# Performance work log

Measured on AMD Instinct MI355X. Metric: run time of the kernel, lower is better.

The kernel has to match this reference:

```python
import jax, jax.numpy as jnp
import numpy as np

N = 100000
E = 1600000
IN = 128
H = 256
K = 7          # n_hops + 1
INTERVAL = 3
R = K - INTERVAL + 1  # n_relations + 1 = 5


def setup_inputs() -> dict:
    key = jax.random.key(0)
    ks = jax.random.split(key, 8)
    features = jax.random.normal(ks[0], (N, IN), dtype=jnp.float32)
    W1 = jax.random.normal(ks[1], (K, IN, H), dtype=jnp.float32) * (1.0 / np.sqrt(IN))
    b1 = jnp.zeros((K, H), dtype=jnp.float32)
    W2 = jax.random.normal(ks[2], (K, H, H), dtype=jnp.float32) * (1.0 / np.sqrt(H))
    b2 = jnp.zeros((K, H), dtype=jnp.float32)
    Wr = jax.random.normal(ks[3], (R, H * INTERVAL, H), dtype=jnp.float32) * (1.0 / np.sqrt(H * INTERVAL))
    br = jnp.zeros((R, H), dtype=jnp.float32)
    row = jax.random.randint(ks[4], (E,), 0, N, dtype=jnp.int64)
    col = jax.random.randint(ks[5], (E,), 0, N, dtype=jnp.int64)
    return {"features": features, "W1": W1, "b1": b1, "W2": W2, "b2": b2,
            "Wr": Wr, "br": br, "row": row, "col": col}


def _norm_adj(row, col):
    # set_diag=True: add self loops; symm_norm: D^-1/2 (A+I) D^-1/2
    diag = jnp.arange(N, dtype=row.dtype)
    r = jnp.concatenate([row, diag])
    c = jnp.concatenate([col, diag])
    deg = jax.ops.segment_sum(jnp.ones_like(r, dtype=jnp.float32), r, num_segments=N)
    dinv = jnp.where(deg > 0, jax.lax.rsqrt(deg), 0.0)
    w = dinv[r] * dinv[c]  # [E+N]
    return r, c, w


def _forward(features, W1, b1, W2, b2, Wr, br, row, col):
    r, c, w = _norm_adj(row, col)

    def spmm(x):  # x: [N, F] -> A_hat @ x
        return jax.ops.segment_sum(x[c] * w[:, None], r, num_segments=N)

    def step(x, _):
        nx = spmm(x)
        return nx, nx

    _, hops = jax.lax.scan(step, features, None, length=K - 1)  # [K-1, N, IN]
    hop_feats = jnp.concatenate([features[None], hops], axis=0)  # [K, N, IN]

    # per-hop DeepSets (2-layer MLP with ReLU): [K, N, H]
    h = jax.nn.relu(jnp.einsum('kni,kih->knh', hop_feats, W1) + b1[:, None, :])
    h = jnp.einsum('knh,khg->kng', h, W2) + b2[:, None, :]

    hops_feats = jnp.transpose(h, (1, 0, 2))  # [N, K, H]
    # sliding windows of INTERVAL hops: [R, N, INTERVAL*H]
    wins = jnp.stack([hops_feats[:, i:i + INTERVAL, :].reshape(N, INTERVAL * H)
                      for i in range(R)], axis=0)
    rel = jax.nn.relu(jnp.einsum('rnd,rdh->rnh', wins, Wr) + br[:, None, :])  # [R, N, H]
    out = jnp.transpose(rel, (1, 0, 2)).reshape(N, R * H)  # concat over relations
    return out


def reference(features, W1, b1, W2, b2, Wr, br, row, col):
    return _forward(features, W1, b1, W2, b2, Wr, br, row, col)
```

## Files before the change

kernel.cpp:

```cpp
#include <hip/hip_runtime.h>

#define N_NODES 100000
#define E_EDGES 1600000
#define IN_F 128
#define H_F 256
#define K_HOPS 7
#define R_REL 5
#define OUT_W (R_REL * H_F)

typedef __attribute__((ext_vector_type(8))) short short8;
typedef __attribute__((ext_vector_type(4))) float f32x4;

#define GLOAD16(g, l) __builtin_amdgcn_global_load_lds( \
    (const __attribute__((address_space(1))) void*)(g), \
    (__attribute__((address_space(3))) void*)(l), 16, 0, 0)


__global__ void zero_int(int* __restrict__ p, int n) {
    int t = blockIdx.x * blockDim.x + threadIdx.x;
    if (t < n) p[t] = 0;
}

__global__ void deg_count(const int* __restrict__ row, int* __restrict__ deg) {
    int e = blockIdx.x * blockDim.x + threadIdx.x;
    if (e < E_EDGES) atomicAdd(&deg[row[e]], 1);
}

__global__ void dinv_compute(const int* __restrict__ deg, float* __restrict__ dinv) {
    int i = blockIdx.x * blockDim.x + threadIdx.x;
    if (i < N_NODES) dinv[i] = rsqrtf((float)(deg[i] + 1));
}

__global__ __launch_bounds__(1024) void exscan_rowptr(const int* __restrict__ deg,
                                                      int* __restrict__ rowptr) {
    __shared__ int wsum[16];
    __shared__ int carry_s;
    const int t = threadIdx.x, lane = t & 63, wv = t >> 6;
    if (t == 0) carry_s = 0;
    __syncthreads();
    for (int base = 0; base < N_NODES; base += 1024) {
        int i = base + t;
        int v = (i < N_NODES) ? deg[i] : 0;
        int x = v;
#pragma unroll
        for (int off = 1; off < 64; off <<= 1) {
            int n = __shfl_up(x, off, 64);
            if (lane >= off) x += n;
        }
        if (lane == 63) wsum[wv] = x;
        __syncthreads();
        if (wv == 0 && lane < 16) {
            int s = wsum[lane];
#pragma unroll
            for (int off = 1; off < 16; off <<= 1) {
                int n = __shfl_up(s, off, 64);
                if (lane >= off) s += n;
            }
            wsum[lane] = s;
        }
        __syncthreads();
        int wbase = (wv == 0) ? 0 : wsum[wv - 1];
        if (i < N_NODES) rowptr[i] = carry_s + wbase + x - v;
        __syncthreads();
        if (t == 1023) carry_s += wsum[15];
        __syncthreads();
    }
    if (threadIdx.x == 0) rowptr[N_NODES] = carry_s;
}

__global__ void csr_scatter(const int* __restrict__ row, const int* __restrict__ col,
                            const float* __restrict__ dinv, const int* __restrict__ rowptr,
                            int* __restrict__ cursor, int* __restrict__ cols2,
                            float* __restrict__ ew) {
    int e = blockIdx.x * blockDim.x + threadIdx.x;
    if (e >= E_EDGES) return;
    int r = row[e], c = col[e];
    int pos = rowptr[r] + atomicAdd(&cursor[r], 1);
    cols2[pos] = c;
    ew[pos] = dinv[r] * dinv[c];
}

__global__ __launch_bounds__(256) void spmm_csr(
    const float2* __restrict__ x, const int* __restrict__ rowptr,
    const int* __restrict__ cols, const float* __restrict__ w,
    const float* __restrict__ dinv, float2* __restrict__ y) {
    const int wave = threadIdx.x >> 6, lane = threadIdx.x & 63;
    const int i = blockIdx.x * 4 + wave;
    if (i >= N_NODES) return;
    const float d = dinv[i];
    float2 xv = x[(size_t)i * 64 + lane];
    float2 acc;
    acc.x = d * d * xv.x;
    acc.y = d * d * xv.y;
    int j = rowptr[i];
    const int e = rowptr[i + 1];
    for (; j + 3 < e; j += 4) {
        int c0 = cols[j], c1 = cols[j + 1], c2 = cols[j + 2], c3 = cols[j + 3];
        float w0 = w[j], w1 = w[j + 1], w2 = w[j + 2], w3 = w[j + 3];
        float2 v0 = x[(size_t)c0 * 64 + lane];
        float2 v1 = x[(size_t)c1 * 64 + lane];
        float2 v2 = x[(size_t)c2 * 64 + lane];
        float2 v3 = x[(size_t)c3 * 64 + lane];
        acc.x += w0 * v0.x + w1 * v1.x + w2 * v2.x + w3 * v3.x;
        acc.y += w0 * v0.y + w1 * v1.y + w2 * v2.y + w3 * v3.y;
    }
    for (; j < e; ++j) {
        int c0 = cols[j];
        float w0 = w[j];
        float2 v0 = x[(size_t)c0 * 64 + lane];
        acc.x += w0 * v0.x;
        acc.y += w0 * v0.y;
    }
    y[(size_t)i * 64 + lane] = acc;
}


__device__ __forceinline__ void f2bf_split(float v, short& h, short& l) {
    unsigned u = __float_as_uint(v);
    unsigned hb = (u + 0x7FFFu + ((u >> 16) & 1u)) >> 16;
    float fh = __uint_as_float(hb << 16);
    float r = v - fh;
    unsigned u2 = __float_as_uint(r);
    unsigned lb = (u2 + 0x7FFFu + ((u2 >> 16) & 1u)) >> 16;
    h = (short)(unsigned short)hb;
    l = (short)(unsigned short)lb;
}

__global__ __launch_bounds__(256) void wc_compute(const float* __restrict__ W2,
                                                  const float* __restrict__ Wr,
                                                  float* __restrict__ Wc) {
    const int z = blockIdx.x, j = blockIdx.y, g = threadIdx.x;
    const int r = z / 3, d = z % 3, hop = r + d;
    const float* a = W2 + (size_t)hop * H_F * H_F + (size_t)j * H_F;
    const float* b = Wr + ((size_t)r * 768 + (size_t)d * H_F) * H_F + g;
    float acc = 0.f;
#pragma unroll 4
    for (int h = 0; h < H_F; ++h) acc += a[h] * b[(size_t)h * H_F];
    Wc[(size_t)z * H_F * H_F + (size_t)j * H_F + g] = acc;
}

__global__ __launch_bounds__(256) void bc_compute(const float* __restrict__ b2,
                                                  const float* __restrict__ Wr,
                                                  const float* __restrict__ br,
                                                  float* __restrict__ bc) {
    const int r = blockIdx.x, g = threadIdx.x;
    float acc = br[(size_t)r * H_F + g];
    for (int t = 0; t < 3 * H_F; ++t) {
        float bv = b2[(size_t)(r + t / H_F) * H_F + (t % H_F)];
        acc += bv * Wr[((size_t)r * 768 + t) * H_F + g];
    }
    bc[(size_t)r * H_F + g] = acc;
}

__global__ void transpose_convert(const float* __restrict__ in, short* __restrict__ oh,
                                  short* __restrict__ ol, int Kd, int grp) {
    __shared__ float t[32][33];
    const int i0 = blockIdx.x * 32, n0 = blockIdx.y * 32, z = blockIdx.z;
    const int tx = threadIdx.x, ty = threadIdx.y;
    const int outLd = grp * Kd;
    const float* ip = in + (size_t)z * Kd * 256;
#pragma unroll
    for (int j = 0; j < 4; ++j)
        t[ty + 8 * j][tx] = ip[(size_t)(i0 + ty + 8 * j) * 256 + n0 + tx];
    __syncthreads();
    size_t base = (size_t)(z / grp) * 256 * outLd + (size_t)(z % grp) * Kd;
#pragma unroll
    for (int j = 0; j < 4; ++j) {
        float v = t[tx][ty + 8 * j];
        short hb, lb;
        f2bf_split(v, hb, lb);
        size_t o = base + (size_t)(n0 + ty + 8 * j) * outLd + i0 + tx;
        oh[o] = hb;
        ol[o] = lb;
    }
}


#define LROW 40

__global__ __launch_bounds__(256, 2) void gemm_mlp(
    const float* __restrict__ A,
    const short* __restrict__ BTh, const short* __restrict__ BTl,
    short* __restrict__ Ch, short* __restrict__ Cl,
    const float* __restrict__ bias, int M)
{
    __shared__ short lds_buf[4 * 128 * LROW];
    short* Ah = lds_buf;
    short* Al = lds_buf + 128 * LROW;
    short* Bh = lds_buf + 2 * 128 * LROW;
    short* Bl = lds_buf + 3 * 128 * LROW;

    const int tid = threadIdx.x;
    const int lane = tid & 63, wave = tid >> 6;
    const int wm = wave & 1, wn = wave >> 1;
    const int fr = lane & 15, fg = lane >> 4;
    const int m0 = blockIdx.y * 128;
    const int n0 = blockIdx.x * 128;

    const int sr = tid >> 1;
    const int sc = (tid & 1) * 16;
    const bool avalid = (m0 + sr) < M;
    const int arow = avalid ? (m0 + sr) : (M - 1);

    f32x4 ga[4];
    short8 gbh[2], gbl[2];
    {
        const float* ap = A + (size_t)arow * IN_F + sc;
        const short* bph = BTh + (size_t)(n0 + sr) * IN_F + sc;
        const short* bpl = BTl + (size_t)(n0 + sr) * IN_F + sc;
#pragma unroll
        for (int l = 0; l < 4; ++l) ga[l] = *(const f32x4*)(ap + 4 * l);
        gbh[0] = *(const short8*)bph;  gbh[1] = *(const short8*)(bph + 8);
        gbl[0] = *(const short8*)bpl;  gbl[1] = *(const short8*)(bpl + 8);
    }

    f32x4 acc[4][4];
#pragma unroll
    for (int i = 0; i < 4; ++i)
#pragma unroll
        for (int j = 0; j < 4; ++j) acc[i][j] = (f32x4)0.f;

    const int nk = IN_F / 32;
    for (int kk = 0; kk < nk; ++kk) {
        __syncthreads();
        {
            short8 vh[2], vl[2];
#pragma unroll
            for (int l = 0; l < 4; ++l) {
                f32x4 v = ga[l];
                if (!avalid) v = (f32x4)0.f;
#pragma unroll
                for (int e = 0; e < 4; ++e) {
                    short hb, lb;
                    f2bf_split(v[e], hb, lb);
                    vh[l >> 1][(l & 1) * 4 + e] = hb;
                    vl[l >> 1][(l & 1) * 4 + e] = lb;
                }
            }
            *(short8*)(Ah + sr * LROW + sc)     = vh[0];
            *(short8*)(Ah + sr * LROW + sc + 8) = vh[1];
            *(short8*)(Al + sr * LROW + sc)     = vl[0];
            *(short8*)(Al + sr * LROW + sc + 8) = vl[1];
            *(short8*)(Bh + sr * LROW + sc)     = gbh[0];
            *(short8*)(Bh + sr * LROW + sc + 8) = gbh[1];
            *(short8*)(Bl + sr * LROW + sc)     = gbl[0];
            *(short8*)(Bl + sr * LROW + sc + 8) = gbl[1];
        }
        __syncthreads();

        if (kk + 1 < nk) {
            int k0 = (kk + 1) * 32;
            const float* ap = A + (size_t)arow * IN_F + k0 + sc;
            const short* bph = BTh + (size_t)(n0 + sr) * IN_F + k0 + sc;
            const short* bpl = BTl + (size_t)(n0 + sr) * IN_F + k0 + sc;
#pragma unroll
            for (int l = 0; l < 4; ++l) ga[l] = *(const f32x4*)(ap + 4 * l);
            gbh[0] = *(const short8*)bph;  gbh[1] = *(const short8*)(bph + 8);
            gbl[0] = *(const short8*)bpl;  gbl[1] = *(const short8*)(bpl + 8);
        }

        short8 afh[4], afl[4], bfh[4], bfl[4];
#pragma unroll
        for (int mf = 0; mf < 4; ++mf) {
            int r = wm * 64 + mf * 16 + fr;
            afh[mf] = *(const short8*)(Ah + r * LROW + fg * 8);
            afl[mf] = *(const short8*)(Al + r * LROW + fg * 8);
        }
#pragma unroll
        for (int nf = 0; nf < 4; ++nf) {
            int r = wn * 64 + nf * 16 + fr;
            bfh[nf] = *(const short8*)(Bh + r * LROW + fg * 8);
            bfl[nf] = *(const short8*)(Bl + r * LROW + fg * 8);
        }
#pragma unroll
        for (int mf = 0; mf < 4; ++mf)
#pragma unroll
            for (int nf = 0; nf < 4; ++nf) {
                acc[mf][nf] = __builtin_amdgcn_mfma_f32_16x16x32_bf16(
                    afh[mf], bfh[nf], acc[mf][nf], 0, 0, 0);
                acc[mf][nf] = __builtin_amdgcn_mfma_f32_16x16x32_bf16(
                    afh[mf], bfl[nf], acc[mf][nf], 0, 0, 0);
                acc[mf][nf] = __builtin_amdgcn_mfma_f32_16x16x32_bf16(
                    afl[mf], bfh[nf], acc[mf][nf], 0, 0, 0);
            }
    }

#pragma unroll
    for (int nf = 0; nf < 4; ++nf) {
        int colg = n0 + wn * 64 + nf * 16 + fr;
        float bv = bias[colg];
#pragma unroll
        for (int mf = 0; mf < 4; ++mf) {
            int rowbase = m0 + wm * 64 + mf * 16 + fg * 4;
#pragma unroll
            for (int j = 0; j < 4; ++j) {
                int rowg = rowbase + j;
                if (rowg < M) {
                    float v = fmaxf(acc[mf][nf][j] + bv, 0.f);
                    short hb, lb;
                    f2bf_split(v, hb, lb);
                    size_t idx = (size_t)rowg * H_F + colg;
                    Ch[idx] = hb;
                    Cl[idx] = lb;
                }
            }
        }
    }
}


__global__ __launch_bounds__(256, 2) void gemm_rel(
    const short* __restrict__ h1h, const short* __restrict__ h1l, long hopStride,
    const short* __restrict__ wch, const short* __restrict__ wcl,
    float* __restrict__ outB, const float* __restrict__ bcB, int M)
{
    __shared__ short lds[2][4][128 * 32];

    const int tid = threadIdx.x;
    const int lane = tid & 63, wave = tid >> 6;
    const int wm = wave & 1, wn = wave >> 1;
    const int fr = lane & 15, fg = lane >> 4;
    const int m0 = blockIdx.y * 128;
    const int n0 = blockIdx.x * 128;
    const int rrel = blockIdx.z;

    const short* Agh = h1h + (size_t)rrel * hopStride;
    const short* Agl = h1l + (size_t)rrel * hopStride;
    const short* BTh = wch + (size_t)rrel * 256 * 768;
    const short* BTl = wcl + (size_t)rrel * 256 * 768;
    float* C = outB + (size_t)rrel * H_F;
    const float* bias = bcB + (size_t)rrel * H_F;

    int aoff[2], boff[2], loff[2];
#pragma unroll
    for (int q = 0; q < 2; ++q) {
        int c = wave * 2 + q;
        int r = c * 16 + (lane >> 2);
        int u = lane & 3;
        int g = (u - (r >> 1)) & 3;
        int ar = m0 + r; if (ar >= M) ar = M - 1;
        aoff[q] = ar * H_F + g * 8;
        boff[q] = (n0 + r) * 768 + g * 8;
        loff[q] = c * 512;
    }

#define STAGE_REL(buf, kg) do {                                                  \
        int hop_ = (kg) >> 8, kin_ = (kg) & 255;                                 \
        const short* ah_ = Agh + (size_t)hop_ * hopStride + kin_;                \
        const short* al_ = Agl + (size_t)hop_ * hopStride + kin_;                \
        const short* bh_ = BTh + (kg);                                           \
        const short* bl_ = BTl + (kg);                                           \
        GLOAD16(ah_ + aoff[0], &lds[buf][0][loff[0]]);                           \
        GLOAD16(ah_ + aoff[1], &lds[buf][0][loff[1]]);                           \
        GLOAD16(al_ + aoff[0], &lds[buf][1][loff[0]]);                           \
        GLOAD16(al_ + aoff[1], &lds[buf][1][loff[1]]);                           \
        GLOAD16(bh_ + boff[0], &lds[buf][2][loff[0]]);                           \
        GLOAD16(bh_ + boff[1], &lds[buf][2][loff[1]]);                           \
        GLOAD16(bl_ + boff[0], &lds[buf][3][loff[0]]);                           \
        GLOAD16(bl_ + boff[1], &lds[buf][3][loff[1]]);                           \
    } while (0)

    f32x4 acc[4][4];
#pragma unroll
    for (int i = 0; i < 4; ++i)
#pragma unroll
        for (int j = 0; j < 4; ++j) acc[i][j] = (f32x4)0.f;

    STAGE_REL(0, 0);
    __syncthreads();

    int cur = 0;
    const int nk = 768 / 32;
    for (int kt = 0; kt < nk; ++kt) {
        if (kt + 1 < nk) STAGE_REL(cur ^ 1, (kt + 1) * 32);

        const short* Ahc = &lds[cur][0][0];
        const short* Alc = &lds[cur][1][0];
        const short* Bhc = &lds[cur][2][0];
        const short* Blc = &lds[cur][3][0];

        short8 bfh[4], bfl[4];
#pragma unroll
        for (int nf = 0; nf < 4; ++nf) {
            int rb = wn * 64 + nf * 16 + fr;
            int ub = (fg + (rb >> 1)) & 3;
            bfh[nf] = *(const short8*)(Bhc + rb * 32 + ub * 8);
            bfl[nf] = *(const short8*)(Blc + rb * 32 + ub * 8);
        }
#pragma unroll
        for (int mf = 0; mf < 4; ++mf) {
            int ra = wm * 64 + mf * 16 + fr;
            int ua = (fg + (ra >> 1)) & 3;
            short8 ah = *(const short8*)(Ahc + ra * 32 + ua * 8);
            short8 al = *(const short8*)(Alc + ra * 32 + ua * 8);
#pragma unroll
            for (int nf = 0; nf < 4; ++nf) {
                acc[mf][nf] = __builtin_amdgcn_mfma_f32_16x16x32_bf16(
                    ah, bfh[nf], acc[mf][nf], 0, 0, 0);
                acc[mf][nf] = __builtin_amdgcn_mfma_f32_16x16x32_bf16(
                    ah, bfl[nf], acc[mf][nf], 0, 0, 0);
                acc[mf][nf] = __builtin_amdgcn_mfma_f32_16x16x32_bf16(
                    al, bfh[nf], acc[mf][nf], 0, 0, 0);
            }
        }
        __syncthreads();
        cur ^= 1;
    }

#pragma unroll
    for (int nf = 0; nf < 4; ++nf) {
        int colg = n0 + wn * 64 + nf * 16 + fr;
        float bv = bias[colg];
#pragma unroll
        for (int mf = 0; mf < 4; ++mf) {
            int rowbase = m0 + wm * 64 + mf * 16 + fg * 4;
#pragma unroll
            for (int j = 0; j < 4; ++j) {
                int rowg = rowbase + j;
                if (rowg < M)
                    C[(size_t)rowg * OUT_W + colg] = fmaxf(acc[mf][nf][j] + bv, 0.f);
            }
        }
    }
#undef STAGE_REL
}


template <int MODE>
__global__ __launch_bounds__(256, 2) void gemm_presplit(
    const short* __restrict__ Agh, const short* __restrict__ Agl, int lda,
    const short* __restrict__ BTh, const short* __restrict__ BTl, int ldb, int Kd,
    float* __restrict__ C, int ldc, const float* __restrict__ bias, int M)
{
    __shared__ short lds_buf[4 * 128 * LROW];
    short* Ah = lds_buf;
    short* Al = lds_buf + 128 * LROW;
    short* Bh = lds_buf + 2 * 128 * LROW;
    short* Bl = lds_buf + 3 * 128 * LROW;

    const int tid = threadIdx.x;
    const int lane = tid & 63, wave = tid >> 6;
    const int wm = wave & 1, wn = wave >> 1;
    const int fr = lane & 15, fg = lane >> 4;
    const int m0 = blockIdx.y * 128;
    const int n0 = blockIdx.x * 128;

    const int sr = tid >> 1;
    const int sc = (tid & 1) * 16;
    const bool avalid = (m0 + sr) < M;
    const int arow = avalid ? (m0 + sr) : (M - 1);

    short8 gah[2], gal[2], gbh[2], gbl[2];
    {
        const short* aph = Agh + (size_t)arow * lda + sc;
        const short* apl = Agl + (size_t)arow * lda + sc;
        const short* bph = BTh + (size_t)(n0 + sr) * ldb + sc;
        const short* bpl = BTl + (size_t)(n0 + sr) * ldb + sc;
        gah[0] = *(const short8*)aph;  gah[1] = *(const short8*)(aph + 8);
        gal[0] = *(const short8*)apl;  gal[1] = *(const short8*)(apl + 8);
        gbh[0] = *(const short8*)bph;  gbh[1] = *(const short8*)(bph + 8);
        gbl[0] = *(const short8*)bpl;  gbl[1] = *(const short8*)(bpl + 8);
    }

    f32x4 acc[4][4];
#pragma unroll
    for (int i = 0; i < 4; ++i)
#pragma unroll
        for (int j = 0; j < 4; ++j) acc[i][j] = (f32x4)0.f;

    const int nk = Kd / 32;
    for (int kk = 0; kk < nk; ++kk) {
        __syncthreads();
        *(short8*)(Ah + sr * LROW + sc)     = gah[0];
        *(short8*)(Ah + sr * LROW + sc + 8) = gah[1];
        *(short8*)(Al + sr * LROW + sc)     = gal[0];
        *(short8*)(Al + sr * LROW + sc + 8) = gal[1];
        *(short8*)(Bh + sr * LROW + sc)     = gbh[0];
        *(short8*)(Bh + sr * LROW + sc + 8) = gbh[1];
        *(short8*)(Bl + sr * LROW + sc)     = gbl[0];
        *(short8*)(Bl + sr * LROW + sc + 8) = gbl[1];
        __syncthreads();

        if (kk + 1 < nk) {
            int k0 = (kk + 1) * 32;
            const short* aph = Agh + (size_t)arow * lda + k0 + sc;
            const short* apl = Agl + (size_t)arow * lda + k0 + sc;
            const short* bph = BTh + (size_t)(n0 + sr) * ldb + k0 + sc;
            const short* bpl = BTl + (size_t)(n0 + sr) * ldb + k0 + sc;
            gah[0] = *(const short8*)aph;  gah[1] = *(const short8*)(aph + 8);
            gal[0] = *(const short8*)apl;  gal[1] = *(const short8*)(apl + 8);
            gbh[0] = *(const short8*)bph;  gbh[1] = *(const short8*)(bph + 8);
            gbl[0] = *(const short8*)bpl;  gbl[1] = *(const short8*)(bpl + 8);
        }

        short8 afh[4], afl[4], bfh[4], bfl[4];
#pragma unroll
        for (int mf = 0; mf < 4; ++mf) {
            int r = wm * 64 + mf * 16 + fr;
            afh[mf] = *(const short8*)(Ah + r * LROW + fg * 8);
            afl[mf] = *(const short8*)(Al + r * LROW + fg * 8);
        }
#pragma unroll
        for (int nf = 0; nf < 4; ++nf) {
            int r = wn * 64 + nf * 16 + fr;
            bfh[nf] = *(const short8*)(Bh + r * LROW + fg * 8);
            bfl[nf] = *(const short8*)(Bl + r * LROW + fg * 8);
        }
#pragma unroll
        for (int mf = 0; mf < 4; ++mf)
#pragma unroll
            for (int nf = 0; nf < 4; ++nf) {
                acc[mf][nf] = __builtin_amdgcn_mfma_f32_16x16x32_bf16(
                    afh[mf], bfh[nf], acc[mf][nf], 0, 0, 0);
                acc[mf][nf] = __builtin_amdgcn_mfma_f32_16x16x32_bf16(
                    afh[mf], bfl[nf], acc[mf][nf], 0, 0, 0);
                acc[mf][nf] = __builtin_amdgcn_mfma_f32_16x16x32_bf16(
                    afl[mf], bfh[nf], acc[mf][nf], 0, 0, 0);
            }
    }

#pragma unroll
    for (int nf = 0; nf < 4; ++nf) {
        int colg = n0 + wn * 64 + nf * 16 + fr;
        float bv = (MODE == 0) ? bias[colg] : 0.f;
#pragma unroll
        for (int mf = 0; mf < 4; ++mf) {
            int rowbase = m0 + wm * 64 + mf * 16 + fg * 4;
#pragma unroll
            for (int j = 0; j < 4; ++j) {
                int rowg = rowbase + j;
                if (rowg < M) {
                    size_t idx = (size_t)rowg * ldc + colg;
                    float v = acc[mf][nf][j] + bv;
                    if (MODE >= 2) v += C[idx];
                    if (MODE & 1) v = fmaxf(v, 0.f);
                    C[idx] = v;
                }
            }
        }
    }
}


extern "C" void kernel_launch(void* const* d_in, const int* in_sizes, int n_in,
                              void* d_out, int out_size, void* d_ws, size_t ws_size,
                              hipStream_t stream) {
    const float* features = (const float*)d_in[0];
    const float* W1 = (const float*)d_in[1];
    const float* b1 = (const float*)d_in[2];
    const float* W2 = (const float*)d_in[3];
    const float* b2 = (const float*)d_in[4];
    const float* Wr = (const float*)d_in[5];
    const float* br = (const float*)d_in[6];
    const int* row = (const int*)d_in[7];
    const int* col = (const int*)d_in[8];
    float* out = (float*)d_out;

    char* ws = (char*)d_ws;
    int* deg = (int*)ws;
    int* rowptr = (int*)(ws + (1ull << 20));
    float* dinv = (float*)(ws + (2ull << 20));
    int* cols2 = (int*)(ws + (4ull << 20));
    float* ew = (float*)(ws + (11ull << 20));
    short* w1h = (short*)(ws + (18ull << 20));
    short* w1l = (short*)(ws + (19ull << 20));
    float* wc32 = (float*)(ws + (20ull << 20));
    short* wch = (short*)(ws + (24ull << 20));
    short* wcl = (short*)(ws + (26ull << 20));
    float* bc = (float*)(ws + (28ull << 20));
    float* xa = (float*)(ws + (32ull << 20));
    float* xb = (float*)(ws + (96ull << 20));
    short* h1h = (short*)(ws + (160ull << 20));
    short* h1l = (short*)(ws + (576ull << 20));

    const bool windowed = ws_size >= (1000ull << 20);

    zero_int<<<(N_NODES + 255) / 256, 256, 0, stream>>>(deg, N_NODES);
    deg_count<<<(E_EDGES + 255) / 256, 256, 0, stream>>>(row, deg);
    dinv_compute<<<(N_NODES + 255) / 256, 256, 0, stream>>>(deg, dinv);
    exscan_rowptr<<<1, 1024, 0, stream>>>(deg, rowptr);
    zero_int<<<(N_NODES + 255) / 256, 256, 0, stream>>>(deg, N_NODES);
    csr_scatter<<<(E_EDGES + 255) / 256, 256, 0, stream>>>(row, col, dinv, rowptr,
                                                           deg, cols2, ew);

    wc_compute<<<dim3(15, H_F), 256, 0, stream>>>(W2, Wr, wc32);
    bc_compute<<<R_REL, 256, 0, stream>>>(b2, Wr, br, bc);

    dim3 tb(32, 8);
    transpose_convert<<<dim3(IN_F / 32, 8, K_HOPS), tb, 0, stream>>>(W1, w1h, w1l, IN_F, 1);
    transpose_convert<<<dim3(H_F / 32, 8, 15), tb, 0, stream>>>(wc32, wch, wcl, H_F, 3);

    const float* xcur = features;
    float* bufs[2] = {xa, xb};
    for (int k = 0; k < K_HOPS; ++k) {
        short* h1hd = windowed ? (h1h + (size_t)k * N_NODES * H_F) : h1h;
        short* h1ld = windowed ? (h1l + (size_t)k * N_NODES * H_F) : h1l;
        dim3 grid(2, (N_NODES + 127) / 128);
        gemm_mlp<<<grid, 256, 0, stream>>>(xcur, w1h + (size_t)k * 256 * IN_F,
                                           w1l + (size_t)k * 256 * IN_F,
                                           h1hd, h1ld, b1 + (size_t)k * H_F, N_NODES);

        if (!windowed) {
            int rlo = (k - 2 < 0) ? 0 : (k - 2);
            int rhi = (k < R_REL - 1) ? k : (R_REL - 1);
            for (int r = rlo; r <= rhi; ++r) {
                int d = k - r;
                const short* Bh = wch + (size_t)r * 256 * 768 + (size_t)d * H_F;
                const short* Bl = wcl + (size_t)r * 256 * 768 + (size_t)d * H_F;
                float* Cp = out + (size_t)r * H_F;
                if (k == r)
                    gemm_presplit<0><<<grid, 256, 0, stream>>>(
                        h1h, h1l, H_F, Bh, Bl, 768, H_F, Cp, OUT_W,
                        bc + (size_t)r * H_F, N_NODES);
                else if (k == r + 2)
                    gemm_presplit<3><<<grid, 256, 0, stream>>>(
                        h1h, h1l, H_F, Bh, Bl, 768, H_F, Cp, OUT_W, nullptr, N_NODES);
                else
                    gemm_presplit<2><<<grid, 256, 0, stream>>>(
                        h1h, h1l, H_F, Bh, Bl, 768, H_F, Cp, OUT_W, nullptr, N_NODES);
            }
        }

        if (k < K_HOPS - 1) {
            float* xn = bufs[k & 1];
            spmm_csr<<<(N_NODES + 3) / 4, 256, 0, stream>>>(
                (const float2*)xcur, rowptr, cols2, ew, dinv, (float2*)xn);
            xcur = xn;
        }
    }

    if (windowed) {
        dim3 grid(2, (N_NODES + 127) / 128, R_REL);
        gemm_rel<<<grid, 256, 0, stream>>>(h1h, h1l, (long)N_NODES * H_F,
                                           wch, wcl, out, bc, N_NODES);
    }
}
```

Before: 2.437 ms.

## Parallelize rowptr scan across blocks and remap gemm_rel workgroups per XCD

Replaces the single-block serial exclusive scan over node degrees with a three-kernel multi-block scan: per-block partial scans, a tiny serial pass over the block sums, then an add-back pass. It also flattens the gemm_rel 3D grid into a 1D grid and remaps block IDs so that consecutive logical tiles (both N halves and all relations of an M block) land on the same XCD, aiming to improve L2 reuse of the shared A rows. The cost is two extra kernel launches for the scan and some index arithmetic in the GEMM.

```diff
diff --git a/kernel.cpp b/kernel.cpp
--- a/kernel.cpp
+++ b/kernel.cpp
@@ -7,6 +7,7 @@
 #define K_HOPS 7
 #define R_REL 5
 #define OUT_W (R_REL * H_F)
+#define SCAN_B ((N_NODES + 1023) / 1024)
 
 typedef __attribute__((ext_vector_type(8))) short short8;
 typedef __attribute__((ext_vector_type(4))) float f32x4;
@@ -31,41 +32,48 @@
     if (i < N_NODES) dinv[i] = rsqrtf((float)(deg[i] + 1));
 }
 
-__global__ __launch_bounds__(1024) void exscan_rowptr(const int* __restrict__ deg,
-                                                      int* __restrict__ rowptr) {
-    __shared__ int wsum[16];
-    __shared__ int carry_s;
+__global__ __launch_bounds__(1024) void scan1(const int* __restrict__ deg,
+                                              int* __restrict__ rp, int* __restrict__ bsum) {
+    __shared__ int ws[16];
     const int t = threadIdx.x, lane = t & 63, wv = t >> 6;
-    if (t == 0) carry_s = 0;
+    int i = blockIdx.x * 1024 + t;
+    int v = (i < N_NODES) ? deg[i] : 0;
+    int x = v;
+#pragma unroll
+    for (int off = 1; off < 64; off <<= 1) {
+        int n = __shfl_up(x, off, 64);
+        if (lane >= off) x += n;
+    }
+    if (lane == 63) ws[wv] = x;
     __syncthreads();
-    for (int base = 0; base < N_NODES; base += 1024) {
-        int i = base + t;
-        int v = (i < N_NODES) ? deg[i] : 0;
-        int x = v;
-#pragma unroll
-        for (int off = 1; off < 64; off <<= 1) {
-            int n = __shfl_up(x, off, 64);
-            if (lane >= off) x += n;
-        }
-        if (lane == 63) wsum[wv] = x;
-        __syncthreads();
-        if (wv == 0 && lane < 16) {
-            int s = wsum[lane];
-#pragma unroll
-            for (int off = 1; off < 16; off <<= 1) {
-                int n = __shfl_up(s, off, 64);
-                if (lane >= off) s += n;
-            }
-            wsum[lane] = s;
-        }
-        __syncthreads();
-        int wbase = (wv == 0) ? 0 : wsum[wv - 1];
-        if (i < N_NODES) rowptr[i] = carry_s + wbase + x - v;
-        __syncthreads();
-        if (t == 1023) carry_s += wsum[15];
-        __syncthreads();
-    }
-    if (threadIdx.x == 0) rowptr[N_NODES] = carry_s;
+    if (wv == 0 && lane < 16) {
+        int s = ws[lane];
+#pragma unroll
+        for (int off = 1; off < 16; off <<= 1) {
+            int n = __shfl_up(s, off, 64);
+            if (lane >= off) s += n;
+        }
+        ws[lane] = s;
+    }
+    __syncthreads();
+    int wbase = (wv == 0) ? 0 : ws[wv - 1];
+    if (i < N_NODES) rp[i] = wbase + x - v;
+    if (t == 1023) bsum[blockIdx.x] = ws[15];
+}
+
+__global__ void scan2(int* __restrict__ bsum) {
+    if (threadIdx.x == 0 && blockIdx.x == 0) {
+        int acc = 0;
+        for (int b = 0; b < SCAN_B; ++b) { int v = bsum[b]; bsum[b] = acc; acc += v; }
+        bsum[SCAN_B] = acc;
+    }
+}
+
+__global__ __launch_bounds__(1024) void scan3(int* __restrict__ rp,
+                                              const int* __restrict__ bsum) {
+    int i = blockIdx.x * 1024 + threadIdx.x;
+    if (i < N_NODES) rp[i] += bsum[blockIdx.x];
+    if (i == 0) rp[N_NODES] = bsum[SCAN_B];
 }
 
 __global__ void csr_scatter(const int* __restrict__ row, const int* __restrict__ col,
@@ -255,8 +263,8 @@
             const short* bpl = BTl + (size_t)(n0 + sr) * IN_F + k0 + sc;
 #pragma unroll
             for (int l = 0; l < 4; ++l) ga[l] = *(const f32x4*)(ap + 4 * l);
-            gbh[0] = *(const short8*)bph;  gbh[1] = *(const short8*)(bph + 8);
-            gbl[0] = *(const short8*)bpl;  gbl[1] = *(const short8*)(bpl + 8);
+            gbh[0] = *(const short8*)(bph);  gbh[1] = *(const short8*)(bph + 8);
+            gbl[0] = *(const short8*)(bpl);  gbl[1] = *(const short8*)(bpl + 8);
         }
 
         short8 afh[4], afl[4], bfh[4], bfl[4];
@@ -312,17 +320,25 @@
 __global__ __launch_bounds__(256, 2) void gemm_rel(
     const short* __restrict__ h1h, const short* __restrict__ h1l, long hopStride,
     const short* __restrict__ wch, const short* __restrict__ wcl,
-    float* __restrict__ outB, const float* __restrict__ bcB, int M)
+    float* __restrict__ outB, const float* __restrict__ bcB, int M, int nwg)
 {
     __shared__ short lds[2][4][128 * 32];
+
+    const int bid = blockIdx.x;
+    const int q8 = nwg >> 3, r8 = nwg & 7;
+    const int xcd = bid & 7, idx = bid >> 3;
+    const int wgid = (xcd < r8) ? (xcd * (q8 + 1) + idx)
+                                : (r8 * (q8 + 1) + (xcd - r8) * q8 + idx);
+    const int q = wgid % 10;
+    const int mblk = wgid / 10;
+    const int n0 = (q & 1) * 128;
+    const int rrel = q >> 1;
+    const int m0 = mblk * 128;
 
     const int tid = threadIdx.x;
     const int lane = tid & 63, wave = tid >> 6;
     const int wm = wave & 1, wn = wave >> 1;
     const int fr = lane & 15, fg = lane >> 4;
-    const int m0 = blockIdx.y * 128;
-    const int n0 = blockIdx.x * 128;
-    const int rrel = blockIdx.z;
 
     const short* Agh = h1h + (size_t)rrel * hopStride;
     const short* Agl = h1l + (size_t)rrel * hopStride;
@@ -333,15 +349,15 @@
 
     int aoff[2], boff[2], loff[2];
 #pragma unroll
-    for (int q = 0; q < 2; ++q) {
-        int c = wave * 2 + q;
+    for (int p = 0; p < 2; ++p) {
+        int c = wave * 2 + p;
         int r = c * 16 + (lane >> 2);
         int u = lane & 3;
         int g = (u - (r >> 1)) & 3;
         int ar = m0 + r; if (ar >= M) ar = M - 1;
-        aoff[q] = ar * H_F + g * 8;
-        boff[q] = (n0 + r) * 768 + g * 8;
-        loff[q] = c * 512;
+        aoff[p] = ar * H_F + g * 8;
+        boff[p] = (n0 + r) * 768 + g * 8;
+        loff[p] = c * 512;
     }
 
 #define STAGE_REL(buf, kg) do {                                                  \
@@ -560,6 +576,7 @@
     int* deg = (int*)ws;
     int* rowptr = (int*)(ws + (1ull << 20));
     float* dinv = (float*)(ws + (2ull << 20));
+    int* bsum = (int*)(ws + (3ull << 20));
     int* cols2 = (int*)(ws + (4ull << 20));
     float* ew = (float*)(ws + (11ull << 20));
     short* w1h = (short*)(ws + (18ull << 20));
@@ -578,7 +595,9 @@
     zero_int<<<(N_NODES + 255) / 256, 256, 0, stream>>>(deg, N_NODES);
     deg_count<<<(E_EDGES + 255) / 256, 256, 0, stream>>>(row, deg);
     dinv_compute<<<(N_NODES + 255) / 256, 256, 0, stream>>>(deg, dinv);
-    exscan_rowptr<<<1, 1024, 0, stream>>>(deg, rowptr);
+    scan1<<<SCAN_B, 1024, 0, stream>>>(deg, rowptr, bsum);
+    scan2<<<1, 64, 0, stream>>>(bsum);
+    scan3<<<SCAN_B, 1024, 0, stream>>>(rowptr, bsum);
     zero_int<<<(N_NODES + 255) / 256, 256, 0, stream>>>(deg, N_NODES);
     csr_scatter<<<(E_EDGES + 255) / 256, 256, 0, stream>>>(row, col, dinv, rowptr,
                                                            deg, cols2, ew);
@@ -630,8 +649,9 @@
     }
 
     if (windowed) {
-        dim3 grid(2, (N_NODES + 127) / 128, R_REL);
-        gemm_rel<<<grid, 256, 0, stream>>>(h1h, h1l, (long)N_NODES * H_F,
-                                           wch, wcl, out, bc, N_NODES);
-    }
-}
+        int mblocks = (N_NODES + 127) / 128;
+        int nwg = mblocks * 2 * R_REL;
+        gemm_rel<<<nwg, 256, 0, stream>>>(h1h, h1l, (long)N_NODES * H_F,
+                                          wch, wcl, out, bc, N_NODES, nwg);
+    }
+}
```

New measurement: 2.331 ms. 4.4% less time.
